# Kernel optimization log

Hardware: AMD Instinct MI355X
Metric: run time of the kernel (lower is better)

## Reference

```python
import jax, jax.numpy as jnp
import numpy as np

# DMoAH constants (match init_kwargs)
H_TOTAL = 16   # attn_h_total
H_ACTIVE = 4   # attn_h_active (per-token top-k heads)


def setup_inputs() -> dict:
    key = jax.random.key(0)
    k1, k2, k3, k4 = jax.random.split(key, 4)
    B, T, D = 2, 2048, 1024
    x = jax.random.normal(k1, (B, T, D), dtype=jnp.float32)
    W_qkv = jax.random.normal(k2, (D, 3 * D), dtype=jnp.float32) * (1.0 / np.sqrt(D))
    W_router = jax.random.normal(k3, (D, H_TOTAL), dtype=jnp.float32) * (1.0 / np.sqrt(D))
    W_o = jax.random.normal(k4, (D, D), dtype=jnp.float32) * (1.0 / np.sqrt(D))
    return {"x": x, "W_qkv": W_qkv, "W_router": W_router, "W_o": W_o}


def reference(x, W_qkv, W_router, W_o):
    B, T, D = x.shape
    dh = D // H_TOTAL
    # --- router: per-token softmax over heads, keep top-k head probs (others zeroed) ---
    probs = jax.nn.softmax(x @ W_router, axis=-1)                 # [B,T,H]
    topv, _ = jax.lax.top_k(probs, H_ACTIVE)                      # [B,T,k]
    thresh = topv[..., -1:]                                       # kth largest prob
    gates = jnp.where(probs >= thresh, probs, 0.0)                # [B,T,H] sparse gates
    # --- QKV projection ---
    qkv = x @ W_qkv                                               # [B,T,3D]
    q, k, v = jnp.split(qkv, 3, axis=-1)
    q = q.reshape(B, T, H_TOTAL, dh).transpose(0, 2, 1, 3)        # [B,H,T,dh]
    k = k.reshape(B, T, H_TOTAL, dh).transpose(0, 2, 1, 3)
    v = v.reshape(B, T, H_TOTAL, dh).transpose(0, 2, 1, 3)
    # --- causal SDPA per head ---
    scale = 1.0 / np.sqrt(dh).astype(np.float32)
    scores = jnp.einsum("bhqd,bhkd->bhqk", q, k) * scale          # [B,H,T,T]
    causal = jnp.tril(jnp.ones((T, T), dtype=bool))
    scores = jnp.where(causal, scores, -jnp.inf)
    attn = jax.nn.softmax(scores, axis=-1)
    head_out = jnp.einsum("bhqk,bhkd->bhqd", attn, v)             # [B,H,T,dh]
    # --- per-token head gating (scatter-combine of active heads) ---
    head_out = head_out.transpose(0, 2, 1, 3)                     # [B,T,H,dh]
    y = (head_out * gates[..., None]).reshape(B, T, D)
    return y @ W_o
```

## Files before the change

kernel.cpp:

```cpp
#include <hip/hip_runtime.h>
#include <math.h>

#define BB 2
#define TT 2048
#define DD 1024
#define HH 16
#define DH 64
#define BTOT (BB*TT)
#define NEG_INF (-1e30f)
#define V_LO 0

typedef _Float16 half8 __attribute__((ext_vector_type(8)));
typedef _Float16 half4 __attribute__((ext_vector_type(4)));
typedef float floatx4 __attribute__((ext_vector_type(4)));

__global__ __launch_bounds__(256) void split_f32(const float* __restrict__ in,
                                                 _Float16* __restrict__ hi,
                                                 _Float16* __restrict__ lo,
                                                 int n4) {
  int idx = blockIdx.x * 256 + threadIdx.x;
  const int stride = gridDim.x * 256;
  for (; idx < n4; idx += stride) {
    float4 v = reinterpret_cast<const float4*>(in)[idx];
    half4 hv, lv;
    hv[0] = (_Float16)v.x; lv[0] = (_Float16)(v.x - (float)hv[0]);
    hv[1] = (_Float16)v.y; lv[1] = (_Float16)(v.y - (float)hv[1]);
    hv[2] = (_Float16)v.z; lv[2] = (_Float16)(v.z - (float)hv[2]);
    hv[3] = (_Float16)v.w; lv[3] = (_Float16)(v.w - (float)hv[3]);
    reinterpret_cast<half4*>(hi)[idx] = hv;
    reinterpret_cast<half4*>(lo)[idx] = lv;
  }
}

__global__ __launch_bounds__(256) void wsplit_t(const float* __restrict__ W,
                                                _Float16* __restrict__ Wth,
                                                _Float16* __restrict__ Wtl,
                                                int K, int N) {
  __shared__ float buf[64][65];
  const int tid = threadIdx.x;
  const int k0 = blockIdx.y * 64;
  const int n0 = blockIdx.x * 64;
  const int rr = tid >> 4;
  const int cc = (tid & 15) * 4;
#pragma unroll
  for (int p = 0; p < 4; ++p) {
    const int r = rr + p * 16;
    float4 v = *reinterpret_cast<const float4*>(&W[(size_t)(k0 + r) * N + n0 + cc]);
    buf[r][cc+0] = v.x; buf[r][cc+1] = v.y; buf[r][cc+2] = v.z; buf[r][cc+3] = v.w;
  }
  __syncthreads();
  const int tn = tid >> 2;
#pragma unroll
  for (int pp = 0; pp < 2; ++pp) {
    const int c2 = (tid & 3) + pp * 4;
    half8 hv, lv;
#pragma unroll
    for (int j = 0; j < 8; ++j) {
      float f = buf[c2*8 + j][tn];
      hv[j] = (_Float16)f;
      lv[j] = (_Float16)(f - (float)hv[j]);
    }
    *reinterpret_cast<half8*>(&Wth[(size_t)(n0 + tn) * K + k0 + c2*8]) = hv;
    *reinterpret_cast<half8*>(&Wtl[(size_t)(n0 + tn) * K + k0 + c2*8]) = lv;
  }
}

__global__ __launch_bounds__(64) void router_kernel(const float* __restrict__ x,
                                                    const float* __restrict__ Wr,
                                                    float* __restrict__ gates) {
  const int row = blockIdx.x;
  const int lane = threadIdx.x;
  const float* xr = x + (size_t)row * DD;
  float acc[16];
#pragma unroll
  for (int c = 0; c < 16; ++c) acc[c] = 0.f;
  for (int d = lane; d < DD; d += 64) {
    float xv = xr[d];
    const float4* wrow = reinterpret_cast<const float4*>(Wr + (size_t)d * HH);
#pragma unroll
    for (int g = 0; g < 4; ++g) {
      float4 w = wrow[g];
      acc[g*4+0] = fmaf(xv, w.x, acc[g*4+0]);
      acc[g*4+1] = fmaf(xv, w.y, acc[g*4+1]);
      acc[g*4+2] = fmaf(xv, w.z, acc[g*4+2]);
      acc[g*4+3] = fmaf(xv, w.w, acc[g*4+3]);
    }
  }
#pragma unroll
  for (int c = 0; c < 16; ++c) {
    float v = acc[c];
    v += __shfl_down(v, 32);
    v += __shfl_down(v, 16);
    v += __shfl_down(v, 8);
    v += __shfl_down(v, 4);
    v += __shfl_down(v, 2);
    v += __shfl_down(v, 1);
    acc[c] = v;
  }
  if (lane == 0) {
    float mx = acc[0];
#pragma unroll
    for (int c = 1; c < 16; ++c) mx = fmaxf(mx, acc[c]);
    float e[16]; float den = 0.f;
#pragma unroll
    for (int c = 0; c < 16; ++c) { e[c] = __expf(acc[c] - mx); den += e[c]; }
    float tmp[16];
#pragma unroll
    for (int c = 0; c < 16; ++c) tmp[c] = acc[c];
    float th = NEG_INF;
    for (int it = 0; it < 4; ++it) {
      float bv = NEG_INF; int bi = 0;
      for (int c = 0; c < 16; ++c) { if (tmp[c] > bv) { bv = tmp[c]; bi = c; } }
      tmp[bi] = NEG_INF;
      th = bv;
    }
    float inv = 1.f / den;
    float* gr = gates + (size_t)row * HH;
#pragma unroll
    for (int c = 0; c < 16; ++c) gr[c] = (acc[c] >= th) ? e[c] * inv : 0.f;
  }
}

template<bool EMIT_HALF>
__global__ __launch_bounds__(256) void hgemm_split(const _Float16* __restrict__ Ah,
                                                   const _Float16* __restrict__ Al,
                                                   const _Float16* __restrict__ Bth,
                                                   const _Float16* __restrict__ Btl,
                                                   float* __restrict__ C,
                                                   _Float16* __restrict__ Ch,
                                                   _Float16* __restrict__ Cl,
                                                   int M, int N, int K) {
  __shared__ _Float16 As[2][128][40];
  __shared__ _Float16 Bs[2][128][40];
  const int tid = threadIdx.x;
  const int lane = tid & 63;
  const int w = tid >> 6;
  const int wr = w >> 1, wc = w & 1;
  const int lr = lane & 15, lg = lane >> 4;
  const int m0 = blockIdx.y * 128, n0 = blockIdx.x * 128;
  const int srow = tid >> 2;
  const int schunk = (tid & 3) * 8;
  const _Float16* ApH = Ah + (size_t)(m0 + srow) * K + schunk;
  const _Float16* ApL = Al + (size_t)(m0 + srow) * K + schunk;
  const _Float16* BpH = Bth + (size_t)(n0 + srow) * K + schunk;
  const _Float16* BpL = Btl + (size_t)(n0 + srow) * K + schunk;
  const size_t rskip = (size_t)64 * K;

  floatx4 acc[4][4] = {};
  for (int k0 = 0; k0 < K; k0 += 32) {
    int4 a0h = *reinterpret_cast<const int4*>(ApH + k0);
    int4 a1h = *reinterpret_cast<const int4*>(ApH + rskip + k0);
    int4 a0l = *reinterpret_cast<const int4*>(ApL + k0);
    int4 a1l = *reinterpret_cast<const int4*>(ApL + rskip + k0);
    int4 b0h = *reinterpret_cast<const int4*>(BpH + k0);
    int4 b1h = *reinterpret_cast<const int4*>(BpH + rskip + k0);
    int4 b0l = *reinterpret_cast<const int4*>(BpL + k0);
    int4 b1l = *reinterpret_cast<const int4*>(BpL + rskip + k0);
    __syncthreads();
    *reinterpret_cast<int4*>(&As[0][srow][schunk])      = a0h;
    *reinterpret_cast<int4*>(&As[0][srow + 64][schunk]) = a1h;
    *reinterpret_cast<int4*>(&As[1][srow][schunk])      = a0l;
    *reinterpret_cast<int4*>(&As[1][srow + 64][schunk]) = a1l;
    *reinterpret_cast<int4*>(&Bs[0][srow][schunk])      = b0h;
    *reinterpret_cast<int4*>(&Bs[0][srow + 64][schunk]) = b1h;
    *reinterpret_cast<int4*>(&Bs[1][srow][schunk])      = b0l;
    *reinterpret_cast<int4*>(&Bs[1][srow + 64][schunk]) = b1l;
    __syncthreads();
    half8 af[2][4], bf[2][4];
#pragma unroll
    for (int mi = 0; mi < 4; ++mi) {
      af[0][mi] = *reinterpret_cast<const half8*>(&As[0][wr*64 + mi*16 + lr][lg*8]);
      af[1][mi] = *reinterpret_cast<const half8*>(&As[1][wr*64 + mi*16 + lr][lg*8]);
    }
#pragma unroll
    for (int ni = 0; ni < 4; ++ni) {
      bf[0][ni] = *reinterpret_cast<const half8*>(&Bs[0][wc*64 + ni*16 + lr][lg*8]);
      bf[1][ni] = *reinterpret_cast<const half8*>(&Bs[1][wc*64 + ni*16 + lr][lg*8]);
    }
#pragma unroll
    for (int mi = 0; mi < 4; ++mi)
#pragma unroll
      for (int ni = 0; ni < 4; ++ni) {
        acc[mi][ni] = __builtin_amdgcn_mfma_f32_16x16x32_f16(af[0][mi], bf[0][ni], acc[mi][ni], 0, 0, 0);
        acc[mi][ni] = __builtin_amdgcn_mfma_f32_16x16x32_f16(af[0][mi], bf[1][ni], acc[mi][ni], 0, 0, 0);
        acc[mi][ni] = __builtin_amdgcn_mfma_f32_16x16x32_f16(af[1][mi], bf[0][ni], acc[mi][ni], 0, 0, 0);
      }
  }
#pragma unroll
  for (int mi = 0; mi < 4; ++mi)
#pragma unroll
    for (int ni = 0; ni < 4; ++ni) {
      const int n = n0 + wc*64 + ni*16 + lr;
#pragma unroll
      for (int r = 0; r < 4; ++r) {
        const int m = m0 + wr*64 + mi*16 + lg*4 + r;
        const float v = acc[mi][ni][r];
        if (EMIT_HALF) {
          const _Float16 vh = (_Float16)v;
          Ch[(size_t)m * N + n] = vh;
          Cl[(size_t)m * N + n] = (_Float16)(v - (float)vh);
        } else {
          C[(size_t)m * N + n] = v;
        }
      }
    }
}

__global__ __launch_bounds__(256) void attn_mfma(const _Float16* __restrict__ qkvh,
                                                 const _Float16* __restrict__ qkvl,
                                                 const float* __restrict__ gates,
                                                 _Float16* __restrict__ yhi,
                                                 _Float16* __restrict__ ylo) {
  __shared__ _Float16 Ksh[64][68], Ksl[64][68];
  __shared__ _Float16 Vth[64][68];
#if V_LO
  __shared__ _Float16 Vtl[64][68];
#endif
  __shared__ _Float16 Psh[64][68], Psl[64][68];
  const int nQT = TT / 64;
  const int bid = blockIdx.x;
  const int qt = nQT - 1 - bid / (BB*HH);
  const int bh = bid % (BB*HH);
  const int b = bh / HH, h = bh % HH;
  const int tid = threadIdx.x;
  const int lane = tid & 63;
  const int wv = tid >> 6;
  const int lr = lane & 15;
  const int lg = lane >> 4;
  const size_t rs = 3 * DD;
  const _Float16* kbh = qkvh + (size_t)b*TT*rs + DD + h*DH;
  const _Float16* kbl = qkvl + (size_t)b*TT*rs + DD + h*DH;
  const _Float16* vbh = qkvh + (size_t)b*TT*rs + 2*DD + h*DH;
#if V_LO
  const _Float16* vbl = qkvl + (size_t)b*TT*rs + 2*DD + h*DH;
#endif

  half8 qfh[2], qfl[2];
  {
    const _Float16* qrh = qkvh + (size_t)(b*TT + qt*64 + wv*16 + lr) * rs + h*DH + lg*8;
    const _Float16* qrl = qkvl + (size_t)(b*TT + qt*64 + wv*16 + lr) * rs + h*DH + lg*8;
#pragma unroll
    for (int c = 0; c < 2; ++c) {
      qfh[c] = *reinterpret_cast<const half8*>(qrh + c*32);
      qfl[c] = *reinterpret_cast<const half8*>(qrl + c*32);
    }
  }
  floatx4 oacc[4] = {};
  float rowM[4], rowL[4];
#pragma unroll
  for (int r = 0; r < 4; ++r) { rowM[r] = NEG_INF; rowL[r] = 0.f; }

  const int sm = tid >> 2;
  const int sg = tid & 3;

  for (int jt = 0; jt <= qt; ++jt) {
    const size_t roff = (size_t)(jt*64 + sm) * rs + sg*16;
    half8 kh0 = *reinterpret_cast<const half8*>(kbh + roff);
    half8 kh1 = *reinterpret_cast<const half8*>(kbh + roff + 8);
    half8 kl0 = *reinterpret_cast<const half8*>(kbl + roff);
    half8 kl1 = *reinterpret_cast<const half8*>(kbl + roff + 8);
    half8 vh0 = *reinterpret_cast<const half8*>(vbh + roff);
    half8 vh1 = *reinterpret_cast<const half8*>(vbh + roff + 8);
#if V_LO
    half8 vl0 = *reinterpret_cast<const half8*>(vbl + roff);
    half8 vl1 = *reinterpret_cast<const half8*>(vbl + roff + 8);
#endif
    __syncthreads();
    *reinterpret_cast<half8*>(&Ksh[sm][sg*16])     = kh0;
    *reinterpret_cast<half8*>(&Ksh[sm][sg*16 + 8]) = kh1;
    *reinterpret_cast<half8*>(&Ksl[sm][sg*16])     = kl0;
    *reinterpret_cast<half8*>(&Ksl[sm][sg*16 + 8]) = kl1;
#pragma unroll
    for (int jj = 0; jj < 8; ++jj) {
      Vth[sg*16 + jj][sm]     = vh0[jj];
      Vth[sg*16 + 8 + jj][sm] = vh1[jj];
#if V_LO
      Vtl[sg*16 + jj][sm]     = vl0[jj];
      Vtl[sg*16 + 8 + jj][sm] = vl1[jj];
#endif
    }
    __syncthreads();
    floatx4 sacc[4] = {};
#pragma unroll
    for (int c = 0; c < 2; ++c)
#pragma unroll
      for (int nf = 0; nf < 4; ++nf) {
        half8 kfh = *reinterpret_cast<const half8*>(&Ksh[nf*16 + lr][c*32 + lg*8]);
        half8 kfl = *reinterpret_cast<const half8*>(&Ksl[nf*16 + lr][c*32 + lg*8]);
        sacc[nf] = __builtin_amdgcn_mfma_f32_16x16x32_f16(qfh[c], kfh, sacc[nf], 0, 0, 0);
        sacc[nf] = __builtin_amdgcn_mfma_f32_16x16x32_f16(qfh[c], kfl, sacc[nf], 0, 0, 0);
        sacc[nf] = __builtin_amdgcn_mfma_f32_16x16x32_f16(qfl[c], kfh, sacc[nf], 0, 0, 0);
      }
    float p[4][4];
    float corr[4];
#pragma unroll
    for (int r = 0; r < 4; ++r) {
      const int qidx = qt*64 + wv*16 + lg*4 + r;
      float tmax = NEG_INF;
#pragma unroll
      for (int nf = 0; nf < 4; ++nf) {
        const int kidx = jt*64 + nf*16 + lr;
        float sv = sacc[nf][r] * 0.125f;
        if (kidx > qidx) sv = NEG_INF;
        p[nf][r] = sv;
        tmax = fmaxf(tmax, sv);
      }
      tmax = fmaxf(tmax, __shfl_xor(tmax, 1));
      tmax = fmaxf(tmax, __shfl_xor(tmax, 2));
      tmax = fmaxf(tmax, __shfl_xor(tmax, 4));
      tmax = fmaxf(tmax, __shfl_xor(tmax, 8));
      const float mnew = fmaxf(rowM[r], tmax);
      corr[r] = __expf(rowM[r] - mnew);
      float tsum = 0.f;
#pragma unroll
      for (int nf = 0; nf < 4; ++nf) {
        const float pv = __expf(p[nf][r] - mnew);
        p[nf][r] = pv;
        tsum += pv;
      }
      tsum += __shfl_xor(tsum, 1);
      tsum += __shfl_xor(tsum, 2);
      tsum += __shfl_xor(tsum, 4);
      tsum += __shfl_xor(tsum, 8);
      rowL[r] = rowL[r] * corr[r] + tsum;
      rowM[r] = mnew;
    }
#pragma unroll
    for (int nf = 0; nf < 4; ++nf)
#pragma unroll
      for (int r = 0; r < 4; ++r) {
        const _Float16 ph = (_Float16)p[nf][r];
        Psh[wv*16 + lg*4 + r][nf*16 + lr] = ph;
        Psl[wv*16 + lg*4 + r][nf*16 + lr] = (_Float16)(p[nf][r] - (float)ph);
      }
#pragma unroll
    for (int df = 0; df < 4; ++df)
#pragma unroll
      for (int r = 0; r < 4; ++r)
        oacc[df][r] *= corr[r];
#pragma unroll
    for (int c = 0; c < 2; ++c) {
      half8 pah = *reinterpret_cast<const half8*>(&Psh[wv*16 + lr][c*32 + lg*8]);
      half8 pal = *reinterpret_cast<const half8*>(&Psl[wv*16 + lr][c*32 + lg*8]);
#pragma unroll
      for (int df = 0; df < 4; ++df) {
        half8 vfh = *reinterpret_cast<const half8*>(&Vth[df*16 + lr][c*32 + lg*8]);
        oacc[df] = __builtin_amdgcn_mfma_f32_16x16x32_f16(pah, vfh, oacc[df], 0, 0, 0);
        oacc[df] = __builtin_amdgcn_mfma_f32_16x16x32_f16(pal, vfh, oacc[df], 0, 0, 0);
#if V_LO
        half8 vfl = *reinterpret_cast<const half8*>(&Vtl[df*16 + lr][c*32 + lg*8]);
        oacc[df] = __builtin_amdgcn_mfma_f32_16x16x32_f16(pah, vfl, oacc[df], 0, 0, 0);
#endif
      }
    }
  }
#pragma unroll
  for (int r = 0; r < 4; ++r) {
    const int t = qt*64 + wv*16 + lg*4 + r;
    const float g = gates[((size_t)(b*TT + t)) * HH + h];
    const float sc = g / rowL[r];
#pragma unroll
    for (int df = 0; df < 4; ++df) {
      const float v = oacc[df][r] * sc;
      const _Float16 vh = (_Float16)v;
      const size_t off = ((size_t)(b*TT + t)) * DD + h*DH + df*16 + lr;
      yhi[off] = vh;
      ylo[off] = (_Float16)(v - (float)vh);
    }
  }
}

extern "C" void kernel_launch(void* const* d_in, const int* in_sizes, int n_in,
                              void* d_out, int out_size, void* d_ws, size_t ws_size,
                              hipStream_t stream) {
  (void)in_sizes; (void)n_in; (void)out_size; (void)ws_size;
  const float* x    = (const float*)d_in[0];
  const float* Wqkv = (const float*)d_in[1];
  const float* Wr   = (const float*)d_in[2];
  const float* Wo   = (const float*)d_in[3];
  float* out = (float*)d_out;

  _Float16* qkvh = (_Float16*)d_ws;
  _Float16* qkvl = qkvh + (size_t)BTOT * 3 * DD;
  float*    gates = (float*)(qkvl + (size_t)BTOT * 3 * DD);
  _Float16* x_hi = (_Float16*)(gates + (size_t)BTOT * HH);
  _Float16* x_lo = x_hi + (size_t)BTOT * DD;
  _Float16* Wqh  = x_lo + (size_t)BTOT * DD;
  _Float16* Wql  = Wqh + (size_t)DD * 3 * DD;
  _Float16* Woh  = Wql + (size_t)DD * 3 * DD;
  _Float16* Wol  = Woh + (size_t)DD * DD;
  _Float16* yhi = x_hi;
  _Float16* ylo = x_lo;

  split_f32<<<1024, 256, 0, stream>>>(x, x_hi, x_lo, BTOT * DD / 4);
  wsplit_t<<<dim3(3*DD/64, DD/64), 256, 0, stream>>>(Wqkv, Wqh, Wql, DD, 3*DD);
  wsplit_t<<<dim3(DD/64, DD/64), 256, 0, stream>>>(Wo, Woh, Wol, DD, DD);
  router_kernel<<<BTOT, 64, 0, stream>>>(x, Wr, gates);
  hgemm_split<true><<<dim3(3*DD/128, BTOT/128), 256, 0, stream>>>(
      x_hi, x_lo, Wqh, Wql, nullptr, qkvh, qkvl, BTOT, 3*DD, DD);
  attn_mfma<<<(TT/64)*BB*HH, 256, 0, stream>>>(qkvh, qkvl, gates, yhi, ylo);
  hgemm_split<false><<<dim3(DD/128, BTOT/128), 256, 0, stream>>>(
      yhi, ylo, Woh, Wol, out, nullptr, nullptr, BTOT, DD, DD);
}
```

Before: 350.0 us.

## Enlarge attention query tile to 128 rows with 512-thread blocks

The attention kernel now handles 128 query rows per block using 8 waves, so each loaded K/V tile in shared memory serves twice as many queries and global K/V traffic per query drops. Each thread loads half as much per tile. Waves whose rows lie entirely before a key tile skip its compute but still take part in the loads and barriers. The grid shrinks to 512 blocks, and causal load imbalance within a block leaves some waves idle. The unused V_LO path is also removed.

```diff
diff --git a/kernel.cpp b/kernel.cpp
--- a/kernel.cpp
+++ b/kernel.cpp
@@ -8,7 +8,6 @@
 #define DH 64
 #define BTOT (BB*TT)
 #define NEG_INF (-1e30f)
-#define V_LO 0
 
 typedef _Float16 half8 __attribute__((ext_vector_type(8)));
 typedef _Float16 half4 __attribute__((ext_vector_type(4)));
@@ -206,18 +205,15 @@
     }
 }
 
-__global__ __launch_bounds__(256) void attn_mfma(const _Float16* __restrict__ qkvh,
+__global__ __launch_bounds__(512) void attn_mfma(const _Float16* __restrict__ qkvh,
                                                  const _Float16* __restrict__ qkvl,
                                                  const float* __restrict__ gates,
                                                  _Float16* __restrict__ yhi,
                                                  _Float16* __restrict__ ylo) {
   __shared__ _Float16 Ksh[64][68], Ksl[64][68];
   __shared__ _Float16 Vth[64][68];
-#if V_LO
-  __shared__ _Float16 Vtl[64][68];
-#endif
-  __shared__ _Float16 Psh[64][68], Psl[64][68];
-  const int nQT = TT / 64;
+  __shared__ _Float16 Psh[128][68], Psl[128][68];
+  const int nQT = TT / 128;
   const int bid = blockIdx.x;
   const int qt = nQT - 1 - bid / (BB*HH);
   const int bh = bid % (BB*HH);
@@ -231,14 +227,11 @@
   const _Float16* kbh = qkvh + (size_t)b*TT*rs + DD + h*DH;
   const _Float16* kbl = qkvl + (size_t)b*TT*rs + DD + h*DH;
   const _Float16* vbh = qkvh + (size_t)b*TT*rs + 2*DD + h*DH;
-#if V_LO
-  const _Float16* vbl = qkvl + (size_t)b*TT*rs + 2*DD + h*DH;
-#endif
 
   half8 qfh[2], qfl[2];
   {
-    const _Float16* qrh = qkvh + (size_t)(b*TT + qt*64 + wv*16 + lr) * rs + h*DH + lg*8;
-    const _Float16* qrl = qkvl + (size_t)(b*TT + qt*64 + wv*16 + lr) * rs + h*DH + lg*8;
+    const _Float16* qrh = qkvh + (size_t)(b*TT + qt*128 + wv*16 + lr) * rs + h*DH + lg*8;
+    const _Float16* qrl = qkvl + (size_t)(b*TT + qt*128 + wv*16 + lr) * rs + h*DH + lg*8;
 #pragma unroll
     for (int c = 0; c < 2; ++c) {
       qfh[c] = *reinterpret_cast<const half8*>(qrh + c*32);
@@ -250,36 +243,24 @@
 #pragma unroll
   for (int r = 0; r < 4; ++r) { rowM[r] = NEG_INF; rowL[r] = 0.f; }
 
-  const int sm = tid >> 2;
-  const int sg = tid & 3;
-
-  for (int jt = 0; jt <= qt; ++jt) {
-    const size_t roff = (size_t)(jt*64 + sm) * rs + sg*16;
-    half8 kh0 = *reinterpret_cast<const half8*>(kbh + roff);
-    half8 kh1 = *reinterpret_cast<const half8*>(kbh + roff + 8);
-    half8 kl0 = *reinterpret_cast<const half8*>(kbl + roff);
-    half8 kl1 = *reinterpret_cast<const half8*>(kbl + roff + 8);
-    half8 vh0 = *reinterpret_cast<const half8*>(vbh + roff);
-    half8 vh1 = *reinterpret_cast<const half8*>(vbh + roff + 8);
-#if V_LO
-    half8 vl0 = *reinterpret_cast<const half8*>(vbl + roff);
-    half8 vl1 = *reinterpret_cast<const half8*>(vbl + roff + 8);
-#endif
+  const int sm = tid >> 3;
+  const int sg = tid & 7;
+  const int wmax = qt*128 + wv*16 + 15;
+  const int jmax = 2*qt + 1;
+
+  for (int jt = 0; jt <= jmax; ++jt) {
+    const size_t roff = (size_t)(jt*64 + sm) * rs + sg*8;
+    half8 kh = *reinterpret_cast<const half8*>(kbh + roff);
+    half8 kl = *reinterpret_cast<const half8*>(kbl + roff);
+    half8 vh = *reinterpret_cast<const half8*>(vbh + roff);
     __syncthreads();
-    *reinterpret_cast<half8*>(&Ksh[sm][sg*16])     = kh0;
-    *reinterpret_cast<half8*>(&Ksh[sm][sg*16 + 8]) = kh1;
-    *reinterpret_cast<half8*>(&Ksl[sm][sg*16])     = kl0;
-    *reinterpret_cast<half8*>(&Ksl[sm][sg*16 + 8]) = kl1;
-#pragma unroll
-    for (int jj = 0; jj < 8; ++jj) {
-      Vth[sg*16 + jj][sm]     = vh0[jj];
-      Vth[sg*16 + 8 + jj][sm] = vh1[jj];
-#if V_LO
-      Vtl[sg*16 + jj][sm]     = vl0[jj];
-      Vtl[sg*16 + 8 + jj][sm] = vl1[jj];
-#endif
-    }
+    *reinterpret_cast<half8*>(&Ksh[sm][sg*8]) = kh;
+    *reinterpret_cast<half8*>(&Ksl[sm][sg*8]) = kl;
+#pragma unroll
+    for (int jj = 0; jj < 8; ++jj)
+      Vth[sg*8 + jj][sm] = vh[jj];
     __syncthreads();
+    if (jt*64 > wmax) continue;
     floatx4 sacc[4] = {};
 #pragma unroll
     for (int c = 0; c < 2; ++c)
@@ -295,7 +276,7 @@
     float corr[4];
 #pragma unroll
     for (int r = 0; r < 4; ++r) {
-      const int qidx = qt*64 + wv*16 + lg*4 + r;
+      const int qidx = qt*128 + wv*16 + lg*4 + r;
       float tmax = NEG_INF;
 #pragma unroll
       for (int nf = 0; nf < 4; ++nf) {
@@ -347,16 +328,12 @@
         half8 vfh = *reinterpret_cast<const half8*>(&Vth[df*16 + lr][c*32 + lg*8]);
         oacc[df] = __builtin_amdgcn_mfma_f32_16x16x32_f16(pah, vfh, oacc[df], 0, 0, 0);
         oacc[df] = __builtin_amdgcn_mfma_f32_16x16x32_f16(pal, vfh, oacc[df], 0, 0, 0);
-#if V_LO
-        half8 vfl = *reinterpret_cast<const half8*>(&Vtl[df*16 + lr][c*32 + lg*8]);
-        oacc[df] = __builtin_amdgcn_mfma_f32_16x16x32_f16(pah, vfl, oacc[df], 0, 0, 0);
-#endif
       }
     }
   }
 #pragma unroll
   for (int r = 0; r < 4; ++r) {
-    const int t = qt*64 + wv*16 + lg*4 + r;
+    const int t = qt*128 + wv*16 + lg*4 + r;
     const float g = gates[((size_t)(b*TT + t)) * HH + h];
     const float sc = g / rowL[r];
 #pragma unroll
@@ -398,7 +375,7 @@
   router_kernel<<<BTOT, 64, 0, stream>>>(x, Wr, gates);
   hgemm_split<true><<<dim3(3*DD/128, BTOT/128), 256, 0, stream>>>(
       x_hi, x_lo, Wqh, Wql, nullptr, qkvh, qkvl, BTOT, 3*DD, DD);
-  attn_mfma<<<(TT/64)*BB*HH, 256, 0, stream>>>(qkvh, qkvl, gates, yhi, ylo);
+  attn_mfma<<<(TT/128)*BB*HH, 512, 0, stream>>>(qkvh, qkvl, gates, yhi, ylo);
   hgemm_split<false><<<dim3(DD/128, BTOT/128), 256, 0, stream>>>(
       yhi, ylo, Woh, Wol, out, nullptr, nullptr, BTOT, DD, DD);
 }
```

New measurement: 355.7 us. No clear change (+1.6%).
